# Kernel tuning notes

Measured on AMD Instinct MI355X. Metric: run time of the kernel, lower is better.

Reference implementation:

```python
import jax, jax.numpy as jnp
import numpy as np

N_NODES = 100000
N_EDGES = 1600000


def gcn_conv(x, W, b, src, dst, ew, n):
    """PyG GCNConv: x@W, symmetric deg^-1/2 norm with self-loops, scatter-add at dst, +b."""
    loop = jnp.arange(n, dtype=src.dtype)
    s = jnp.concatenate([src, loop])            # sources incl. self-loops
    d = jnp.concatenate([dst, loop])            # targets incl. self-loops
    w = jnp.concatenate([ew, jnp.ones((n,), ew.dtype)])  # self-loop weight = 1
    deg = jax.ops.segment_sum(w, d, num_segments=n)      # weighted in-degree
    dinv = jnp.where(deg > 0, jax.lax.rsqrt(deg), 0.0)
    norm = dinv[s] * w * dinv[d]                # [E+N]
    h = x @ W                                   # [N, F_out]
    msg = h[s] * norm[:, None]                  # gather + per-edge scale
    out = jax.ops.segment_sum(msg, d, num_segments=n)    # scatter-add
    return out + b


def setup_inputs() -> dict:
    key = jax.random.key(0)
    ks = jax.random.split(key, 8)
    in_dim, hid, lat = 128, 128, 64
    x = jax.random.normal(ks[0], (N_NODES, in_dim), jnp.float32)
    edge_index = jax.random.randint(ks[1], (2, N_EDGES), 0, N_NODES, dtype=jnp.int32)
    weights = jax.random.uniform(ks[2], (N_EDGES,), jnp.float32)
    s_in = 1.0 / np.sqrt(in_dim)
    s_h = 1.0 / np.sqrt(hid)
    return {
        "x": x,
        "edge_index": edge_index,
        "weights": weights,
        "W1": jax.random.normal(ks[3], (in_dim, hid), jnp.float32) * s_in,
        "b1": jnp.zeros((hid,), jnp.float32),
        "W2": jax.random.normal(ks[4], (hid, hid), jnp.float32) * s_h,
        "b2": jnp.zeros((hid,), jnp.float32),
        "W_mu": jax.random.normal(ks[5], (hid, lat), jnp.float32) * s_h,
        "b_mu": jnp.zeros((lat,), jnp.float32),
        "W_lv": jax.random.normal(ks[6], (hid, lat), jnp.float32) * s_h,
        "b_lv": jnp.zeros((lat,), jnp.float32),
    }


def reference(x, edge_index, weights, W1, b1, W2, b2, W_mu, b_mu, W_lv, b_lv):
    n = x.shape[0]
    src, dst = edge_index[0], edge_index[1]
    h = jax.nn.relu(gcn_conv(x, W1, b1, src, dst, weights, n))
    h = gcn_conv(h, W2, b2, src, dst, weights, n)
    g = jnp.mean(h, axis=0, keepdims=True)      # [1, hid] global mean pool
    mu = g @ W_mu + b_mu
    logvar = g @ W_lv + b_lv
    return (mu, logvar)
```

## Files before the change

### kernel.cpp

```cpp
#include <hip/hip_runtime.h>


typedef __bf16 bf16x8 __attribute__((ext_vector_type(8)));
typedef float f32x4 __attribute__((ext_vector_type(4)));
typedef float f32x2 __attribute__((ext_vector_type(2)));
typedef unsigned long long u64;

#define NSL 24

__device__ __forceinline__ float bf2f(unsigned short u){
  return __uint_as_float(((unsigned)u) << 16);
}
__device__ __forceinline__ unsigned short f2bf(float f){
  unsigned u = __float_as_uint(f);
  u += 0x7fffu + ((u >> 16) & 1u);
  return (unsigned short)(u >> 16);
}
__device__ __forceinline__ __bf16 us2bf(unsigned short u){
  __bf16 b; __builtin_memcpy(&b, &u, 2); return b;
}
__device__ __forceinline__ float ldf(const void* p, int i, int isf32){
  return isf32 ? ((const float*)p)[i] : bf2f(((const unsigned short*)p)[i]);
}
__device__ __forceinline__ void fma8f8(float* acc, float n, uint2 h){
  f32x2 p0 = __builtin_amdgcn_cvt_pk_f32_fp8((int)h.x, false);
  f32x2 p1 = __builtin_amdgcn_cvt_pk_f32_fp8((int)h.x, true);
  f32x2 p2 = __builtin_amdgcn_cvt_pk_f32_fp8((int)h.y, false);
  f32x2 p3 = __builtin_amdgcn_cvt_pk_f32_fp8((int)h.y, true);
  acc[0] = fmaf(n, p0[0], acc[0]);
  acc[1] = fmaf(n, p0[1], acc[1]);
  acc[2] = fmaf(n, p1[0], acc[2]);
  acc[3] = fmaf(n, p1[1], acc[3]);
  acc[4] = fmaf(n, p2[0], acc[4]);
  acc[5] = fmaf(n, p2[1], acc[5]);
  acc[6] = fmaf(n, p3[0], acc[6]);
  acc[7] = fmaf(n, p3[1], acc[7]);
}
__device__ __forceinline__ void runOfShard(const int* __restrict__ hist, int r, int s,
                                           int lane, int& off, int& len){
  int hv = (lane < 8) ? hist[r * 8 + lane] : 0;
  off = 0; len = 0;
  #pragma unroll
  for (int i = 0; i < 8; ++i){
    int h = __shfl(hv, i);
    if (i < s) off += h;
    if (i == s) len = h;
  }
}

__global__ void k_init(const unsigned* __restrict__ xw, int* __restrict__ flag,
                       const void* __restrict__ W1, unsigned short* __restrict__ W1T,
                       float* __restrict__ v){
  __shared__ int s[256];
  int t = threadIdx.x;
  int cnt = 0;
  for (int k = t; k < 4096; k += 256){
    unsigned lo = xw[k] & 0xFFFFu;
    int e = (int)((lo >> 7) & 0xFFu);
    if ((e >= 100 && e <= 141) || (lo & 0x7FFFu) == 0) cnt++;
  }
  s[t] = cnt;
  __syncthreads();
  for (int off = 128; off > 0; off >>= 1){
    if (t < off) s[t] += s[t + off];
    __syncthreads();
  }
  int isf32 = (s[0] < 2458) ? 1 : 0;
  if (blockIdx.x == 0){
    if (t == 0) *flag = isf32;
    if (t < 128) v[t] = 0.0f;
  }
  int gid = blockIdx.x * 256 + t;
  int k = gid & 127, n = gid >> 7;
  W1T[gid] = isf32 ? f2bf(((const float*)W1)[k * 128 + n])
                   : ((const unsigned short*)W1)[k * 128 + n];
}

__global__ void __launch_bounds__(256) k_binA(const int* __restrict__ src,
    const int* __restrict__ dst, const void* __restrict__ w,
    u64* __restrict__ stagD, u64* __restrict__ stagS,
    int* __restrict__ histD, int* __restrict__ histS,
    int E, int DSv, const int* __restrict__ flagp){
  __shared__ int gcnt[256];
  __shared__ int gincl[256];
  __shared__ u64 bufD[1024];
  __shared__ u64 bufS[1024];
  int tid = threadIdx.x, lane = tid & 63, wv = tid >> 6;
  gcnt[tid] = 0;
  __syncthreads();
  int isf32 = *flagp;
  u64 ltmask = (1ull << lane) - 1ull;
  int sh1v[4], off1v[4], sh2v[4], off2v[4];
  u64 r1v[4], r2v[4];
  #pragma unroll
  for (int k = 0; k < 4; ++k){
    int e = blockIdx.x * 1024 + k * 256 + tid;
    int sh1 = -1, sh2 = -1; u64 r1 = 0, r2 = 0;
    if (e < E){
      int s_ = src[e], d_ = dst[e];
      float wf = ldf(w, e, isf32);
      int nq = (int)(wf * 32768.0f + 0.5f);
      if (nq > 32767) nq = 32767;
      r1 = ((u64)(unsigned)d_ << 32) | ((u64)(unsigned)s_ << 15) | (unsigned)nq;
      r2 = ((u64)(unsigned)s_ << 32) | ((u64)(unsigned)d_ << 15) | (unsigned)nq;
      sh1 = d_ / DSv;
      sh2 = s_ / DSv;
    }
    int o1 = 0, o2 = 0;
    #pragma unroll
    for (int s = 0; s < 8; ++s){
      u64 m1 = __ballot(sh1 == s);
      if (sh1 == s){ o1 = __popcll(m1 & ltmask); if (!o1) gcnt[s * 16 + k * 4 + wv] = __popcll(m1); }
      u64 m2 = __ballot(sh2 == s);
      if (sh2 == s){ o2 = __popcll(m2 & ltmask); if (!o2) gcnt[128 + s * 16 + k * 4 + wv] = __popcll(m2); }
    }
    sh1v[k] = sh1; off1v[k] = o1; r1v[k] = r1;
    sh2v[k] = sh2; off2v[k] = o2; r2v[k] = r2;
  }
  __syncthreads();
  gincl[tid] = gcnt[tid];
  __syncthreads();
  for (int ofs = 1; ofs < 256; ofs <<= 1){
    int t2 = (tid >= ofs) ? gincl[tid - ofs] : 0;
    __syncthreads();
    gincl[tid] += t2;
    __syncthreads();
  }
  int tot1 = gincl[127];
  #pragma unroll
  for (int k = 0; k < 4; ++k){
    if (sh1v[k] >= 0){
      int i1 = sh1v[k] * 16 + k * 4 + wv;
      bufD[gincl[i1] - gcnt[i1] + off1v[k]] = r1v[k];
      int i2 = 128 + sh2v[k] * 16 + k * 4 + wv;
      bufS[gincl[i2] - gcnt[i2] - tot1 + off2v[k]] = r2v[k];
    }
  }
  __syncthreads();
  for (int t = tid; t < tot1; t += 256)
    stagD[(size_t)blockIdx.x * 1024 + t] = bufD[t];
  int tot2 = gincl[255] - tot1;
  for (int t = tid; t < tot2; t += 256)
    stagS[(size_t)blockIdx.x * 1024 + t] = bufS[t];
  if (tid < 8){
    int a  = gincl[tid * 16 + 15];
    int pr = tid ? gincl[tid * 16 - 1] : 0;
    histD[blockIdx.x * 8 + tid] = a - pr;
    int a2  = gincl[128 + tid * 16 + 15];
    int pr2 = gincl[128 + tid * 16 - 1];
    histS[blockIdx.x * 8 + tid] = a2 - pr2;
  }
}

__global__ void __launch_bounds__(256) k_binB(const u64* __restrict__ stagD,
    const int* __restrict__ histD, unsigned* __restrict__ cntdegP,
    int NREG, int per, int DSv){
  __shared__ unsigned cd[12512];
  int tid = threadIdx.x, lane = tid & 63, wv = tid >> 6;
  int s = (int)blockIdx.x & 7, j = (int)blockIdx.x >> 3;
  for (int i = tid; i < DSv; i += 256) cd[i] = 0u;
  __syncthreads();
  int r0 = j * per, r1 = r0 + per;
  if (r1 > NREG) r1 = NREG;
  for (int r = r0 + wv; r < r1; r += 4){
    int off, len;
    runOfShard(histD, r, s, lane, off, len);
    const u64* rp = stagD + (size_t)r * 1024 + off;
    for (int i = lane; i < len; i += 64){
      u64 rec = rp[i];
      int dl = (int)(rec >> 32) - s * DSv;
      if ((unsigned)dl < (unsigned)DSv)
        atomicAdd(&cd[dl], (1u << 20) | (unsigned)((rec & 32767u) >> 2));
    }
  }
  __syncthreads();
  unsigned* op = cntdegP + (size_t)blockIdx.x * DSv;
  for (int i = tid; i < DSv; i += 256) op[i] = cd[i];
}

__global__ void k_scanA(const unsigned* __restrict__ cntdegP, float* __restrict__ dinv,
                        int* __restrict__ cnt, int* __restrict__ rowptr,
                        int* __restrict__ bsum, int N, int DSv){
  __shared__ int sm[256];
  int i = blockIdx.x * 256 + threadIdx.x;
  int val = 0;
  if (i < N){
    int s = i / DSv, local = i - s * DSv;
    unsigned c = 0, dg = 0;
    #pragma unroll
    for (int j = 0; j < NSL; ++j){
      unsigned p = cntdegP[(size_t)(j * 8 + s) * DSv + local];
      c += p >> 20;
      dg += p & 0xFFFFFu;
    }
    dinv[i] = rsqrtf(1.0f + (float)dg * (1.0f / 8192.0f));
    cnt[i] = (int)c;
    val = (int)c;
  }
  sm[threadIdx.x] = val;
  __syncthreads();
  for (int off = 1; off < 256; off <<= 1){
    int tmp = (threadIdx.x >= off) ? sm[threadIdx.x - off] : 0;
    __syncthreads();
    sm[threadIdx.x] += tmp;
    __syncthreads();
  }
  if (i < N) rowptr[i] = sm[threadIdx.x] - val;
  if (threadIdx.x == 255) bsum[blockIdx.x] = sm[255];
}

__global__ void k_scanB(const int* __restrict__ bsum, int* __restrict__ boffs, int NB){
  __shared__ int s[512];
  int t = threadIdx.x;
  int val = (t < NB) ? bsum[t] : 0;
  s[t] = val;
  __syncthreads();
  for (int off = 1; off < 512; off <<= 1){
    int tmp = (t >= off) ? s[t - off] : 0;
    __syncthreads();
    s[t] += tmp;
    __syncthreads();
  }
  boffs[t] = s[t] - val;
}

__global__ void k_scanC(int* __restrict__ rowptr, const int* __restrict__ boffs,
                        const unsigned* __restrict__ cntdegP, int* __restrict__ P,
                        int N, int DSv){
  int i = blockIdx.x * 256 + threadIdx.x;
  if (i >= N) return;
  int rp = rowptr[i] + boffs[blockIdx.x];
  rowptr[i] = rp;
  int s = i / DSv, local = i - s * DSv;
  int run = rp;
  #pragma unroll
  for (int j = 0; j < NSL; ++j){
    P[(size_t)j * N + i] = run;
    run += (int)(cntdegP[(size_t)(j * 8 + s) * DSv + local] >> 20);
  }
}

__global__ void __launch_bounds__(256) k_binC(const u64* __restrict__ stagD,
    const int* __restrict__ histD, const int* __restrict__ P,
    const float* __restrict__ dinv, unsigned* __restrict__ edges,
    int NREG, int per, int N, int DSv, int E){
  __shared__ unsigned cur[12512];
  int tid = threadIdx.x, lane = tid & 63, wv = tid >> 6;
  int s = (int)blockIdx.x & 7, j = (int)blockIdx.x >> 3;
  for (int i = tid; i < DSv; i += 256){
    int node = s * DSv + i;
    cur[i] = (node < N) ? (unsigned)P[(size_t)j * N + node] : 0u;
  }
  __syncthreads();
  int r0 = j * per, r1 = r0 + per;
  if (r1 > NREG) r1 = NREG;
  for (int r = r0 + wv; r < r1; r += 4){
    int off, len;
    runOfShard(histD, r, s, lane, off, len);
    const u64* rp = stagD + (size_t)r * 1024 + off;
    for (int i = lane; i < len; i += 64){
      u64 rec = rp[i];
      int dl = (int)(rec >> 32) - s * DSv;
      if ((unsigned)dl < (unsigned)DSv){
        int srcI = (int)((rec >> 15) & 0x1FFFFu);
        float nrm = dinv[srcI] * ((float)(rec & 32767u) * (1.0f / 32768.0f))
                  * dinv[s * DSv + dl];
        int nq = (int)(nrm * 32768.0f + 0.5f);
        if (nq > 32767) nq = 32767;
        unsigned pos = atomicAdd(&cur[dl], 1u);
        if (pos < (unsigned)E) edges[pos] = ((unsigned)srcI << 15) | (unsigned)nq;
      }
    }
  }
}

__global__ void __launch_bounds__(256) k_cfacB(const u64* __restrict__ stagS,
    const int* __restrict__ histS, const float* __restrict__ dinv,
    float* __restrict__ cfacP, int NREG, int per, int DSv){
  __shared__ float SL[12512];
  int tid = threadIdx.x, lane = tid & 63, wv = tid >> 6;
  int s = (int)blockIdx.x & 7, j = (int)blockIdx.x >> 3;
  for (int i = tid; i < DSv; i += 256) SL[i] = 0.0f;
  __syncthreads();
  int r0 = j * per, r1 = r0 + per;
  if (r1 > NREG) r1 = NREG;
  for (int r = r0 + wv; r < r1; r += 4){
    int off, len;
    runOfShard(histS, r, s, lane, off, len);
    const u64* rp = stagS + (size_t)r * 1024 + off;
    for (int i = lane; i < len; i += 64){
      u64 rec = rp[i];
      int sl_ = (int)(rec >> 32) - s * DSv;
      int d   = (int)((rec >> 15) & 0x1FFFFu);
      float wq = (float)(rec & 32767u) * (1.0f / 32768.0f);
      if ((unsigned)sl_ < (unsigned)DSv)
        atomicAdd(&SL[sl_], wq * dinv[d]);
    }
  }
  __syncthreads();
  float* op = cfacP + (size_t)blockIdx.x * DSv;
  for (int i = tid; i < DSv; i += 256) op[i] = SL[i];
}

__global__ void k_cfacm(const float* __restrict__ cfacP, const float* __restrict__ dinv,
                        const int* __restrict__ rowptr, const int* __restrict__ cnt,
                        float2* __restrict__ dc, int2* __restrict__ rc, int N, int DSv){
  int i = blockIdx.x * 256 + threadIdx.x;
  if (i >= N) return;
  int s = i / DSv, ii = i - s * DSv;
  float S = 0.0f;
  #pragma unroll
  for (int j = 0; j < NSL; ++j)
    S += cfacP[(size_t)(j * 8 + s) * DSv + ii];
  float di = dinv[i];
  dc[i] = make_float2(di * di, di * di + di * S);
  rc[i] = make_int2(rowptr[i], cnt[i]);
}

__global__ void __launch_bounds__(256) k_gemm(const void* __restrict__ xv,
                                              const __bf16* __restrict__ wt,
                                              unsigned char* __restrict__ H, int N,
                                              const int* __restrict__ flagp){
  int wave = (blockIdx.x * blockDim.x + threadIdx.x) >> 6;
  int lane = threadIdx.x & 63;
  int row16 = wave << 4;
  if (row16 >= N) return;
  int isf32 = *flagp;
  int m = lane & 15, q = lane >> 4;
  size_t planeStride = (size_t)N * 32;
  bf16x8 a0, a1, a2, a3;
  if (isf32){
    const float* ap = (const float*)xv + (size_t)(row16 + m) * 128 + q * 8;
    #pragma unroll
    for (int j = 0; j < 8; ++j){
      a0[j] = us2bf(f2bf(ap[j +  0]));
      a1[j] = us2bf(f2bf(ap[j + 32]));
      a2[j] = us2bf(f2bf(ap[j + 64]));
      a3[j] = us2bf(f2bf(ap[j + 96]));
    }
  } else {
    const __bf16* ap = (const __bf16*)xv + (size_t)(row16 + m) * 128 + q * 8;
    a0 = *(const bf16x8*)(ap +  0);
    a1 = *(const bf16x8*)(ap + 32);
    a2 = *(const bf16x8*)(ap + 64);
    a3 = *(const bf16x8*)(ap + 96);
  }
  for (int nt = 0; nt < 8; ++nt){
    const __bf16* bp = wt + (size_t)(nt * 16 + m) * 128 + q * 8;
    bf16x8 b0 = *(const bf16x8*)(bp +  0);
    bf16x8 b1 = *(const bf16x8*)(bp + 32);
    bf16x8 b2 = *(const bf16x8*)(bp + 64);
    bf16x8 b3 = *(const bf16x8*)(bp + 96);
    f32x4 acc = {0.f, 0.f, 0.f, 0.f};
    acc = __builtin_amdgcn_mfma_f32_16x16x32_bf16(a0, b0, acc, 0, 0, 0);
    acc = __builtin_amdgcn_mfma_f32_16x16x32_bf16(a1, b1, acc, 0, 0, 0);
    acc = __builtin_amdgcn_mfma_f32_16x16x32_bf16(a2, b2, acc, 0, 0, 0);
    acc = __builtin_amdgcn_mfma_f32_16x16x32_bf16(a3, b3, acc, 0, 0, 0);
    unsigned char* op = H + (size_t)(nt >> 1) * planeStride
                          + (size_t)(row16 + q * 4) * 32 + (nt & 1) * 16 + m;
    op[0]  = (unsigned char)(__builtin_amdgcn_cvt_pk_fp8_f32(acc[0], acc[0], 0, false) & 0xFF);
    op[32] = (unsigned char)(__builtin_amdgcn_cvt_pk_fp8_f32(acc[1], acc[1], 0, false) & 0xFF);
    op[64] = (unsigned char)(__builtin_amdgcn_cvt_pk_fp8_f32(acc[2], acc[2], 0, false) & 0xFF);
    op[96] = (unsigned char)(__builtin_amdgcn_cvt_pk_fp8_f32(acc[3], acc[3], 0, false) & 0xFF);
  }
}

__global__ void __launch_bounds__(256) k_agg(const unsigned char* __restrict__ H,
    const int2* __restrict__ rc, const float2* __restrict__ dc,
    const unsigned* __restrict__ edges, const void* __restrict__ b1,
    float* __restrict__ v, int N, int nblk, const int* __restrict__ flagp){
  __shared__ float vsh[32];
  int tid = threadIdx.x;
  if (tid < 32) vsh[tid] = 0.0f;
  __syncthreads();
  int isf32 = *flagp;
  int lane = tid & 63;
  int wv = tid >> 6;
  int slot = lane >> 2;
  int q = lane & 3;
  int sl = (blockIdx.x & 7) >> 1;
  int jblk = (int)(blockIdx.x >> 3) * 2 + (blockIdx.x & 1);
  int slotg = (jblk * 4 + wv) * 16 + slot;
  int totslots = (nblk >> 3) * 2 * 4 * 16;
  const unsigned char* Hp = H + (size_t)sl * ((size_t)N * 32);
  int fbase = sl * 32 + q * 8;
  float bx[8];
  #pragma unroll
  for (int j = 0; j < 8; ++j) bx[j] = ldf(b1, fbase + j, isf32);
  float ax[8] = {0,0,0,0,0,0,0,0};
  int d = slotg;
  int2 rcv = make_int2(0, 0); float2 dcv = make_float2(0.f, 0.f);
  uint2 hs = make_uint2(0u, 0u);
  if (d < N){
    rcv = rc[d]; dcv = dc[d];
    hs = *(const uint2*)(Hp + (size_t)d * 32 + q * 8);
  }
  while (d < N){
    int dn = d + totslots;
    int2 rcn = make_int2(0, 0); float2 dcn = make_float2(0.f, 0.f);
    uint2 hsn = make_uint2(0u, 0u);
    if (dn < N){
      rcn = rc[dn]; dcn = dc[dn];
      hsn = *(const uint2*)(Hp + (size_t)dn * 32 + q * 8);
    }
    float acc[8] = {0,0,0,0,0,0,0,0};
    fma8f8(acc, dcv.x, hs);
    int start = rcv.x, len = rcv.y;
    if (len > 0){
      int last = start + len - 1;
      unsigned e0 = edges[start];
      unsigned e1 = edges[(start + 1 < last) ? start + 1 : last];
      unsigned e2 = edges[(start + 2 < last) ? start + 2 : last];
      unsigned e3 = edges[(start + 3 < last) ? start + 3 : last];
      uint2 h0 = *(const uint2*)(Hp + (size_t)(e0 >> 15) * 32 + q * 8);
      uint2 h1 = *(const uint2*)(Hp + (size_t)(e1 >> 15) * 32 + q * 8);
      for (int k = 0; k < len; ++k){
        int a = start + k + 4;
        unsigned en = edges[a < last ? a : last];
        uint2 hn = *(const uint2*)(Hp + (size_t)(e2 >> 15) * 32 + q * 8);
        fma8f8(acc, (float)(e0 & 32767u) * (1.0f / 32768.0f), h0);
        e0 = e1; e1 = e2; e2 = e3; e3 = en;
        h0 = h1; h1 = hn;
      }
    }
    #pragma unroll
    for (int j = 0; j < 8; ++j){
      float rj = fmaxf(acc[j] + bx[j], 0.0f);
      ax[j] = fmaf(dcv.y, rj, ax[j]);
    }
    d = dn; rcv = rcn; dcv = dcn; hs = hsn;
  }
  #pragma unroll
  for (int j = 0; j < 8; ++j){
    ax[j] += __shfl_xor(ax[j], 4);
    ax[j] += __shfl_xor(ax[j], 8);
    ax[j] += __shfl_xor(ax[j], 16);
    ax[j] += __shfl_xor(ax[j], 32);
  }
  if (slot == 0){
    #pragma unroll
    for (int j = 0; j < 8; ++j) atomicAdd(&vsh[q * 8 + j], ax[j]);
  }
  __syncthreads();
  if (tid < 32) atomicAdd(&v[sl * 32 + tid], vsh[tid]);
}

__global__ void __launch_bounds__(128) k_head(const float* __restrict__ v,
    const void* __restrict__ W2, const void* __restrict__ b2,
    const void* __restrict__ Wmu, const void* __restrict__ bmu,
    const void* __restrict__ Wlv, const void* __restrict__ blv,
    void* __restrict__ outv, float invN, const int* __restrict__ flagp){
  __shared__ float gsh[128];
  __shared__ float tsh[128];
  int t = threadIdx.x;
  int isf32 = *flagp;
  gsh[t] = v[t] * invN;
  __syncthreads();
  float acc = ldf(b2, t, isf32);
  for (int k = 0; k < 128; ++k) acc = fmaf(gsh[k], ldf(W2, k * 128 + t, isf32), acc);
  tsh[t] = acc;
  __syncthreads();
  int j = t & 63;
  const void* Wp = (t < 64) ? Wmu : Wlv;
  float o = ldf((t < 64) ? bmu : blv, j, isf32);
  for (int k = 0; k < 128; ++k) o = fmaf(tsh[k], ldf(Wp, k * 64 + j, isf32), o);
  if (isf32) ((float*)outv)[t] = o;
  else       ((unsigned short*)outv)[t] = f2bf(o);
}

extern "C" void kernel_launch(void* const* d_in, const int* in_sizes, int n_in,
                              void* d_out, int out_size, void* d_ws, size_t ws_size,
                              hipStream_t stream) {
  const void* x   = d_in[0];
  const int*  ei  = (const int*)d_in[1];
  const void* w   = d_in[2];
  const void* W1  = d_in[3];
  const void* b1  = d_in[4];
  const void* W2  = d_in[5];
  const void* b2  = d_in[6];
  const void* Wmu = d_in[7];
  const void* bmu = d_in[8];
  const void* Wlv = d_in[9];
  const void* blv = d_in[10];

  const int N = in_sizes[0] / 128;
  const int E = in_sizes[2];
  const int* src = ei;
  const int* dst = ei + E;

  char* wsb = (char*)d_ws;
  size_t off = 0;
  auto alloc = [&](size_t bytes) -> void* {
    off = (off + 255) & ~(size_t)255;
    void* p = wsb + off;
    off += bytes;
    return p;
  };
  const int NREG = (E + 1023) / 1024;
  const int PER  = (NREG + NSL - 1) / NSL;
  const int DSv  = (N + 7) / 8;
  int*   flag     = (int*)  alloc(16);
  float* dinv     = (float*)alloc((size_t)N * 4);
  int*   cnt      = (int*)  alloc((size_t)N * 4);
  int*   rowptr   = (int*)  alloc((size_t)(N + 1) * 4);
  float2* dc      = (float2*)alloc((size_t)N * 8);
  int2*   rc      = (int2*) alloc((size_t)N * 8);
  int*   bsum     = (int*)  alloc(512 * 4);
  int*   boffs    = (int*)  alloc(512 * 4);
  float* v        = (float*)alloc(128 * 4);
  int*   histD    = (int*)  alloc((size_t)NREG * 8 * 4);
  int*   histS    = (int*)  alloc((size_t)NREG * 8 * 4);
  unsigned short* W1T = (unsigned short*)alloc(128 * 128 * 2);
  size_t P_b = (size_t)NSL * N * 4, cfacP_b = (size_t)NSL * 8 * DSv * 4;
  char* regionP = (char*)alloc(P_b > cfacP_b ? P_b : cfacP_b);
  int*   P     = (int*)regionP;
  float* cfacP = (float*)regionP;
  size_t cdg_b = (size_t)NSL * 8 * DSv * 4, edges_b = (size_t)E * 4;
  char* regionE = (char*)alloc(cdg_b > edges_b ? cdg_b : edges_b);
  unsigned* cntdegP = (unsigned*)regionE;
  unsigned* edges   = (unsigned*)regionE;
  size_t stagD_b = (size_t)NREG * 1024 * 8, H_b = (size_t)N * 128;
  char* regionD = (char*)alloc(stagD_b > H_b ? stagD_b : H_b);
  u64*           stagD = (u64*)regionD;
  unsigned char* H     = (unsigned char*)regionD;
  u64* stagS = (u64*)alloc((size_t)NREG * 1024 * 8);
  (void)ws_size; (void)n_in; (void)out_size;

  const int nb_n = (N + 255) / 256;

  k_init<<<64, 256, 0, stream>>>((const unsigned*)x, flag, W1, W1T, v);
  k_binA<<<NREG, 256, 0, stream>>>(src, dst, w, stagD, stagS, histD, histS,
                                   E, DSv, flag);
  k_binB<<<NSL * 8, 256, 0, stream>>>(stagD, histD, cntdegP, NREG, PER, DSv);
  k_scanA<<<nb_n, 256, 0, stream>>>(cntdegP, dinv, cnt, rowptr, bsum, N, DSv);
  k_scanB<<<1, 512, 0, stream>>>(bsum, boffs, nb_n);
  k_scanC<<<nb_n, 256, 0, stream>>>(rowptr, boffs, cntdegP, P, N, DSv);
  k_binC<<<NSL * 8, 256, 0, stream>>>(stagD, histD, P, dinv, edges,
                                      NREG, PER, N, DSv, E);
  k_cfacB<<<NSL * 8, 256, 0, stream>>>(stagS, histS, dinv, cfacP, NREG, PER, DSv);
  k_cfacm<<<nb_n, 256, 0, stream>>>(cfacP, dinv, rowptr, cnt, dc, rc, N, DSv);
  const int nwaves = (N + 15) / 16;
  const int nb_g = (nwaves + 3) / 4;
  k_gemm<<<nb_g, 256, 0, stream>>>(x, (const __bf16*)W1T, H, N, flag);
  const int nb_agg = 2048;
  k_agg<<<nb_agg, 256, 0, stream>>>(H, rc, dc, edges, b1, v, N, nb_agg, flag);
  k_head<<<1, 128, 0, stream>>>(v, W2, b2, Wmu, bmu, Wlv, blv,
                                d_out, 1.0f / (float)N, flag);
}
```

Before: 369.7 us.

## Store H as full 128-byte fp8 rows and aggregate all features per node

The GEMM now writes H as contiguous 128-byte fp8 rows instead of four 32-byte feature planes. The aggregation kernel assigns 8 lanes per destination node, each loading 16 bytes, so every node's edge list is walked once rather than once per plane. The edge array is padded with 16 zero entries so the prefetch no longer needs clamping, and the gather pipeline is deepened by one stage. This cuts repeated edge-index and rowptr reads, at the cost of more registers per thread and fewer blocks.

```diff
diff --git a/kernel.cpp b/kernel.cpp
--- a/kernel.cpp
+++ b/kernel.cpp
@@ -304,7 +304,9 @@
 
 __global__ void k_cfacm(const float* __restrict__ cfacP, const float* __restrict__ dinv,
                         const int* __restrict__ rowptr, const int* __restrict__ cnt,
-                        float2* __restrict__ dc, int2* __restrict__ rc, int N, int DSv){
+                        float2* __restrict__ dc, int2* __restrict__ rc,
+                        unsigned* __restrict__ edges, int E, int N, int DSv){
+  if (blockIdx.x == 0 && threadIdx.x < 16) edges[E + threadIdx.x] = 0u;
   int i = blockIdx.x * 256 + threadIdx.x;
   if (i >= N) return;
   int s = i / DSv, ii = i - s * DSv;
@@ -327,7 +329,6 @@
   if (row16 >= N) return;
   int isf32 = *flagp;
   int m = lane & 15, q = lane >> 4;
-  size_t planeStride = (size_t)N * 32;
   bf16x8 a0, a1, a2, a3;
   if (isf32){
     const float* ap = (const float*)xv + (size_t)(row16 + m) * 128 + q * 8;
@@ -356,93 +357,90 @@
     acc = __builtin_amdgcn_mfma_f32_16x16x32_bf16(a1, b1, acc, 0, 0, 0);
     acc = __builtin_amdgcn_mfma_f32_16x16x32_bf16(a2, b2, acc, 0, 0, 0);
     acc = __builtin_amdgcn_mfma_f32_16x16x32_bf16(a3, b3, acc, 0, 0, 0);
-    unsigned char* op = H + (size_t)(nt >> 1) * planeStride
-                          + (size_t)(row16 + q * 4) * 32 + (nt & 1) * 16 + m;
-    op[0]  = (unsigned char)(__builtin_amdgcn_cvt_pk_fp8_f32(acc[0], acc[0], 0, false) & 0xFF);
-    op[32] = (unsigned char)(__builtin_amdgcn_cvt_pk_fp8_f32(acc[1], acc[1], 0, false) & 0xFF);
-    op[64] = (unsigned char)(__builtin_amdgcn_cvt_pk_fp8_f32(acc[2], acc[2], 0, false) & 0xFF);
-    op[96] = (unsigned char)(__builtin_amdgcn_cvt_pk_fp8_f32(acc[3], acc[3], 0, false) & 0xFF);
+    unsigned char* op = H + (size_t)(row16 + q * 4) * 128 + nt * 16 + m;
+    op[0]   = (unsigned char)(__builtin_amdgcn_cvt_pk_fp8_f32(acc[0], acc[0], 0, false) & 0xFF);
+    op[128] = (unsigned char)(__builtin_amdgcn_cvt_pk_fp8_f32(acc[1], acc[1], 0, false) & 0xFF);
+    op[256] = (unsigned char)(__builtin_amdgcn_cvt_pk_fp8_f32(acc[2], acc[2], 0, false) & 0xFF);
+    op[384] = (unsigned char)(__builtin_amdgcn_cvt_pk_fp8_f32(acc[3], acc[3], 0, false) & 0xFF);
   }
 }
 
 __global__ void __launch_bounds__(256) k_agg(const unsigned char* __restrict__ H,
     const int2* __restrict__ rc, const float2* __restrict__ dc,
     const unsigned* __restrict__ edges, const void* __restrict__ b1,
-    float* __restrict__ v, int N, int nblk, const int* __restrict__ flagp){
-  __shared__ float vsh[32];
+    float* __restrict__ v, int N, int totslots, const int* __restrict__ flagp){
+  __shared__ float vsh[128];
+  __shared__ float bsh[128];
   int tid = threadIdx.x;
-  if (tid < 32) vsh[tid] = 0.0f;
-  __syncthreads();
   int isf32 = *flagp;
+  if (tid < 128){ vsh[tid] = 0.0f; bsh[tid] = ldf(b1, tid, isf32); }
+  __syncthreads();
   int lane = tid & 63;
   int wv = tid >> 6;
-  int slot = lane >> 2;
-  int q = lane & 3;
-  int sl = (blockIdx.x & 7) >> 1;
-  int jblk = (int)(blockIdx.x >> 3) * 2 + (blockIdx.x & 1);
-  int slotg = (jblk * 4 + wv) * 16 + slot;
-  int totslots = (nblk >> 3) * 2 * 4 * 16;
-  const unsigned char* Hp = H + (size_t)sl * ((size_t)N * 32);
-  int fbase = sl * 32 + q * 8;
-  float bx[8];
-  #pragma unroll
-  for (int j = 0; j < 8; ++j) bx[j] = ldf(b1, fbase + j, isf32);
-  float ax[8] = {0,0,0,0,0,0,0,0};
+  int slot = lane >> 3;
+  int q = lane & 7;
+  int slotg = ((int)blockIdx.x * 4 + wv) * 8 + slot;
+  const unsigned char* Hq = H + q * 16;
+  float ax[16];
+  #pragma unroll
+  for (int j = 0; j < 16; ++j) ax[j] = 0.0f;
   int d = slotg;
   int2 rcv = make_int2(0, 0); float2 dcv = make_float2(0.f, 0.f);
-  uint2 hs = make_uint2(0u, 0u);
+  uint4 hs = make_uint4(0u, 0u, 0u, 0u);
   if (d < N){
     rcv = rc[d]; dcv = dc[d];
-    hs = *(const uint2*)(Hp + (size_t)d * 32 + q * 8);
+    hs = *(const uint4*)(Hq + (size_t)d * 128);
   }
   while (d < N){
     int dn = d + totslots;
     int2 rcn = make_int2(0, 0); float2 dcn = make_float2(0.f, 0.f);
-    uint2 hsn = make_uint2(0u, 0u);
+    uint4 hsn = make_uint4(0u, 0u, 0u, 0u);
     if (dn < N){
       rcn = rc[dn]; dcn = dc[dn];
-      hsn = *(const uint2*)(Hp + (size_t)dn * 32 + q * 8);
-    }
-    float acc[8] = {0,0,0,0,0,0,0,0};
-    fma8f8(acc, dcv.x, hs);
+      hsn = *(const uint4*)(Hq + (size_t)dn * 128);
+    }
+    float acc[16];
+    #pragma unroll
+    for (int j = 0; j < 16; ++j) acc[j] = 0.0f;
+    fma8f8(acc,     dcv.x, make_uint2(hs.x, hs.y));
+    fma8f8(acc + 8, dcv.x, make_uint2(hs.z, hs.w));
     int start = rcv.x, len = rcv.y;
     if (len > 0){
-      int last = start + len - 1;
-      unsigned e0 = edges[start];
-      unsigned e1 = edges[(start + 1 < last) ? start + 1 : last];
-      unsigned e2 = edges[(start + 2 < last) ? start + 2 : last];
-      unsigned e3 = edges[(start + 3 < last) ? start + 3 : last];
-      uint2 h0 = *(const uint2*)(Hp + (size_t)(e0 >> 15) * 32 + q * 8);
-      uint2 h1 = *(const uint2*)(Hp + (size_t)(e1 >> 15) * 32 + q * 8);
+      const unsigned* ep = edges + start;
+      unsigned e0 = ep[0], e1 = ep[1], e2 = ep[2], e3 = ep[3];
+      uint4 h0 = *(const uint4*)(Hq + (size_t)(e0 >> 15) * 128);
+      uint4 h1 = *(const uint4*)(Hq + (size_t)(e1 >> 15) * 128);
+      uint4 h2 = *(const uint4*)(Hq + (size_t)(e2 >> 15) * 128);
+      #pragma unroll 2
       for (int k = 0; k < len; ++k){
-        int a = start + k + 4;
-        unsigned en = edges[a < last ? a : last];
-        uint2 hn = *(const uint2*)(Hp + (size_t)(e2 >> 15) * 32 + q * 8);
-        fma8f8(acc, (float)(e0 & 32767u) * (1.0f / 32768.0f), h0);
+        unsigned en = ep[k + 4];
+        uint4 hn = *(const uint4*)(Hq + (size_t)(e3 >> 15) * 128);
+        float wn = (float)(e0 & 32767u) * (1.0f / 32768.0f);
+        fma8f8(acc,     wn, make_uint2(h0.x, h0.y));
+        fma8f8(acc + 8, wn, make_uint2(h0.z, h0.w));
         e0 = e1; e1 = e2; e2 = e3; e3 = en;
-        h0 = h1; h1 = hn;
+        h0 = h1; h1 = h2; h2 = hn;
       }
     }
     #pragma unroll
-    for (int j = 0; j < 8; ++j){
-      float rj = fmaxf(acc[j] + bx[j], 0.0f);
+    for (int j = 0; j < 16; ++j){
+      float rj = fmaxf(acc[j] + bsh[q * 16 + j], 0.0f);
       ax[j] = fmaf(dcv.y, rj, ax[j]);
     }
     d = dn; rcv = rcn; dcv = dcn; hs = hsn;
   }
   #pragma unroll
-  for (int j = 0; j < 8; ++j){
-    ax[j] += __shfl_xor(ax[j], 4);
+  for (int j = 0; j < 16; ++j){
     ax[j] += __shfl_xor(ax[j], 8);
     ax[j] += __shfl_xor(ax[j], 16);
     ax[j] += __shfl_xor(ax[j], 32);
   }
   if (slot == 0){
     #pragma unroll
-    for (int j = 0; j < 8; ++j) atomicAdd(&vsh[q * 8 + j], ax[j]);
-  }
-  __syncthreads();
-  if (tid < 32) atomicAdd(&v[sl * 32 + tid], vsh[tid]);
+    for (int j = 0; j < 16; ++j) atomicAdd(&vsh[q * 16 + j], ax[j]);
+  }
+  __syncthreads();
+  if (tid < 128) atomicAdd(&v[tid], vsh[tid]);
 }
 
 __global__ void __launch_bounds__(128) k_head(const float* __restrict__ v,
@@ -515,7 +513,7 @@
   char* regionP = (char*)alloc(P_b > cfacP_b ? P_b : cfacP_b);
   int*   P     = (int*)regionP;
   float* cfacP = (float*)regionP;
-  size_t cdg_b = (size_t)NSL * 8 * DSv * 4, edges_b = (size_t)E * 4;
+  size_t cdg_b = (size_t)NSL * 8 * DSv * 4, edges_b = (size_t)E * 4 + 64;
   char* regionE = (char*)alloc(cdg_b > edges_b ? cdg_b : edges_b);
   unsigned* cntdegP = (unsigned*)regionE;
   unsigned* edges   = (unsigned*)regionE;
@@ -538,12 +536,13 @@
   k_binC<<<NSL * 8, 256, 0, stream>>>(stagD, histD, P, dinv, edges,
                                       NREG, PER, N, DSv, E);
   k_cfacB<<<NSL * 8, 256, 0, stream>>>(stagS, histS, dinv, cfacP, NREG, PER, DSv);
-  k_cfacm<<<nb_n, 256, 0, stream>>>(cfacP, dinv, rowptr, cnt, dc, rc, N, DSv);
+  k_cfacm<<<nb_n, 256, 0, stream>>>(cfacP, dinv, rowptr, cnt, dc, rc,
+                                    edges, E, N, DSv);
   const int nwaves = (N + 15) / 16;
   const int nb_g = (nwaves + 3) / 4;
   k_gemm<<<nb_g, 256, 0, stream>>>(x, (const __bf16*)W1T, H, N, flag);
-  const int nb_agg = 2048;
-  k_agg<<<nb_agg, 256, 0, stream>>>(H, rc, dc, edges, b1, v, N, nb_agg, flag);
+  const int nb_agg = 1024;
+  k_agg<<<nb_agg, 256, 0, stream>>>(H, rc, dc, edges, b1, v, N, nb_agg * 32, flag);
   k_head<<<1, 128, 0, stream>>>(v, W2, b2, Wmu, bmu, Wlv, blv,
                                 d_out, 1.0f / (float)N, flag);
 }
```

Measured after the change: 374.6 us. Within noise of the previous version (+1.3%).
